# Performance work log

Hardware: AMD Instinct MI355X
Metric: run time of the kernel (lower is better)

Reference implementation:

```python
import jax, jax.numpy as jnp
import numpy as np

INF = 99999.0  # sentinel used by the original torch module


def _dtw_table(x, y):
    """Full (N+1, M+1) DTW DP table, identical math to the torch double loop.

    Row recurrence: r[j+1] = c[j] + min(prev[j+1], prev[j], r[j]).
    Rewritten as the min-plus linear recurrence r[j+1] = min(a[j] + r[j], b[j])
    with a[j] = c[j], b[j] = c[j] + min(prev[j+1], prev[j]), which is
    associative and solved per-row with lax.associative_scan (wavefront-free
    parallelism within each row); rows advance with lax.scan.
    """
    M = y.shape[0]
    dt = x.dtype
    row0 = jnp.full((M + 1,), INF, dtype=dt).at[0].set(0.0)  # dtw[0, :]
    inf1 = jnp.full((1,), INF, dtype=dt)

    def combine(l, r):
        a1, b1 = l
        a2, b2 = r
        return (a1 + a2, jnp.minimum(a2 + b1, b2))

    def step(prev, xi):
        c = (xi - y) ** 2                              # (M,) squared cost
        m = jnp.minimum(prev[1:], prev[:-1])           # min(dtw[i,j+1], dtw[i,j])
        A, B = jax.lax.associative_scan(combine, (c, c + m))
        r = jnp.minimum(A + INF, B)                    # r[0] = INF folded in
        row = jnp.concatenate([inf1, r])               # dtw[i+1, :]
        return row, row

    _, rows = jax.lax.scan(step, row0, x)              # (N, M+1)
    table = jnp.concatenate([row0[None, :], rows], axis=0)
    return jnp.sqrt(table)


def setup_inputs() -> dict:
    key = jax.random.key(0)
    kx, ky = jax.random.split(key)
    N = M = 6144
    x = jax.random.normal(kx, (N,), dtype=jnp.float32)
    y = jax.random.normal(ky, (M,), dtype=jnp.float32)
    return {"x": x, "y": y}


def reference(x, y):
    return _dtw_table(x, y)
```

## Files before the change

kernel.cpp:

```cpp
#include <hip/hip_runtime.h>
#include <math.h>

#define NN    6144
#define MP1   6145
#define FINF  99999.0f

#define R1     8
#define KC1    8
#define WCH1   (KC1 * 64)
#define GCH1   (NN / WCH1)
#define RTS1   8
#define NWS1   (NN / R1)
#define STEPS1 (NWS1 + 63)

#define R2     4
#define KC2    8
#define WCH2   (KC2 * 64)
#define BR     192
#define NBI    (NN / BR)
#define TS2    (BR / R2)
#define STEPS2 (TS2 + 63)

typedef float f4a __attribute__((ext_vector_type(4), aligned(4)));
typedef float f4v __attribute__((ext_vector_type(4), aligned(16)));

__device__ __forceinline__ float readlane_f(float v, int l) {
    return __int_as_float(__builtin_amdgcn_readlane(__float_as_int(v), l));
}
__device__ __forceinline__ float shup1(float v) {
    return __int_as_float(__builtin_amdgcn_update_dpp(
        0, __float_as_int(v), 0x138, 0xF, 0xF, false));
}

__global__ void __launch_bounds__(64, 1) dtw_bnd(const float* __restrict__ x,
                                                 const float* __restrict__ y,
                                                 int* __restrict__ flags,
                                                 float* __restrict__ bnd,
                                                 float* __restrict__ rowb) {
    const int g    = blockIdx.x;
    const int lane = threadIdx.x;
    const int c0   = g * WCH1 + lane * KC1;

    float yv[KC1], cur[KC1];
#pragma unroll
    for (int q = 0; q < KC1; ++q) {
        yv[q]  = y[c0 + q];
        cur[q] = FINF;
    }
    float pl = (c0 == 0) ? 0.0f : FINF;
    float rowval[R1];
#pragma unroll
    for (int r = 0; r < R1; ++r) rowval[r] = FINF;
    float vbuf = FINF, vnext = FINF;

    const float4* x4 = (const float4*)x;
    float4 xwA  = x4[2 * lane];
    float4 xwB  = x4[2 * lane + 1];
    float4 xwAN = x4[2 * (64 + lane)];
    float4 xwBN = x4[2 * (64 + lane) + 1];
    float xcur[R1];
#pragma unroll
    for (int r = 0; r < R1; ++r) xcur[r] = x[r];

    if (g != 0) {
        while (__hip_atomic_load(&flags[(g - 1) * 16], __ATOMIC_ACQUIRE,
                                 __HIP_MEMORY_SCOPE_AGENT) < 1) {
            __builtin_amdgcn_s_sleep(1);
        }
        vnext = bnd[(size_t)(g - 1) * NN + lane];
    }

    for (int s = 0; s < STEPS1; ++s) {
        if (g != GCH1 - 1 && s > 64 && ((s - 64) & (RTS1 - 1)) == 0) {
            if (lane == 0)
                __hip_atomic_store(&flags[g * 16], (s - 64) >> 3,
                                   __ATOMIC_RELEASE, __HIP_MEMORY_SCOPE_AGENT);
        }

        if (g != 0 && s < NWS1 && (s & (RTS1 - 1)) == 0) vbuf = vnext;

        if (g != 0 && (s & (RTS1 - 1)) == RTS1 - 4 && (s + 4) < NWS1) {
            const int want = ((s + 4) >> 3) + 1;
            while (__hip_atomic_load(&flags[(g - 1) * 16], __ATOMIC_ACQUIRE,
                                     __HIP_MEMORY_SCOPE_AGENT) < want) {
                __builtin_amdgcn_s_sleep(1);
            }
            vnext = bnd[(size_t)(g - 1) * NN + (size_t)R1 * (s + 4) + lane];
        }

        float vin[R1];
#pragma unroll
        for (int r = 0; r < R1; ++r) {
            const float up = shup1(rowval[r]);
            const float vb = readlane_f(vbuf, ((s & (RTS1 - 1)) << 3) + r);
            const float l0 = (g == 0) ? FINF : vb;
            vin[r] = (lane == 0) ? l0 : up;
        }

        const int  t      = s - lane;
        const bool active = (t >= 0) && (t < NWS1);
        if (active) {
            float rv[R1], rd[R1];
#pragma unroll
            for (int r = 0; r < R1; ++r) rv[r] = vin[r];

#pragma unroll
            for (int d = 0; d < R1 + KC1 - 1; ++d) {
#pragma unroll
                for (int r = R1 - 1; r >= 0; --r) {
                    const int q = d - r;
                    if (q < 0 || q >= KC1) continue;
                    const float up = (r == 0) ? cur[q] : rv[r - 1];
                    const float dg = (r == 0) ? ((q == 0) ? pl : cur[q - 1])
                                              : rd[r - 1];
                    const float dx = xcur[r] - yv[q];
                    const float nv = dx * dx + fminf(fminf(up, dg), rv[r]);
                    rd[r] = rv[r];
                    rv[r] = nv;
                    if (r == R1 - 1) cur[q] = nv;
                }
            }
#pragma unroll
            for (int r = 0; r < R1; ++r) rowval[r] = rv[r];
            pl = vin[R1 - 1];

            {
                const int tp1 = t + 1;
                const int k   = tp1 / 24;
                if (k * 24 == tp1 && k >= 1 && k <= NBI - 1) {
                    *(f4a*)&rowb[(size_t)k * MP1 + c0 + 1] =
                        (f4a){cur[0], cur[1], cur[2], cur[3]};
                    *(f4a*)&rowb[(size_t)k * MP1 + c0 + 5] =
                        (f4a){cur[4], cur[5], cur[6], cur[7]};
                }
            }
            if (lane == 63) {
                *(f4v*)&bnd[(size_t)g * NN + (size_t)R1 * t] =
                    (f4v){rowval[0], rowval[1], rowval[2], rowval[3]};
                *(f4v*)&bnd[(size_t)g * NN + (size_t)R1 * t + 4] =
                    (f4v){rowval[4], rowval[5], rowval[6], rowval[7]};
            }
        }

        const int sn = s + 1;
        if ((sn & 63) == 0) {
            xwA = xwAN;
            xwB = xwBN;
            int nb = sn + 64 + lane;
            if (nb > NN / 8 - 1) nb = NN / 8 - 1;
            xwAN = x4[2 * nb];
            xwBN = x4[2 * nb + 1];
        }
        const float* xap = (const float*)&xwA;
        const float* xbp = (const float*)&xwB;
#pragma unroll
        for (int r = 0; r < 4; ++r) {
            const float xs = shup1(xcur[r]);
            const float xj = readlane_f(xap[r], sn & 63);
            xcur[r] = (lane == 0) ? xj : xs;
        }
#pragma unroll
        for (int r = 4; r < 8; ++r) {
            const float xs = shup1(xcur[r]);
            const float xj = readlane_f(xbp[r - 4], sn & 63);
            xcur[r] = (lane == 0) ? xj : xs;
        }
    }

    if (g != GCH1 - 1 && lane == 0) {
        __hip_atomic_store(&flags[g * 16], NWS1 >> 3,
                           __ATOMIC_RELEASE, __HIP_MEMORY_SCOPE_AGENT);
    }
}

__global__ void __launch_bounds__(64, 1) dtw_tile(const float* __restrict__ x,
                                                  const float* __restrict__ y,
                                                  const float* __restrict__ bnd,
                                                  const float* __restrict__ rowb,
                                                  float* __restrict__ out) {
    const int bj   = blockIdx.x;
    const int bi   = blockIdx.y;
    const int lane = threadIdx.x;

    __shared__ float left_s[BR];
    __shared__ float top_s[WCH2 + 1];
    __shared__ float xb_s[BR];

#pragma unroll
    for (int k = 0; k < BR / 64; ++k) {
        const int i = 64 * k + lane;
        left_s[i] = (bj == 0) ? FINF
                              : bnd[(size_t)(bj - 1) * NN + BR * bi + i];
        xb_s[i] = x[BR * bi + i];
    }
    for (int c = lane; c < WCH2 + 1; c += 64) {
        float tv;
        if (bi == 0)                tv = (bj == 0 && c == 0) ? 0.0f : FINF;
        else if (c == 0 && bj == 0) tv = FINF;
        else                        tv = rowb[(size_t)bi * MP1 + WCH2 * bj + c];
        top_s[c] = tv;
    }
    __syncthreads();

    const int c0 = WCH2 * bj + KC2 * lane;
    float yv[KC2], cur[KC2];
#pragma unroll
    for (int q = 0; q < KC2; ++q) {
        yv[q]  = y[c0 + q];
        cur[q] = top_s[KC2 * lane + q + 1];
    }
    float pl = top_s[KC2 * lane];
    float rlast[R2];
#pragma unroll
    for (int r = 0; r < R2; ++r) rlast[r] = FINF;

    float xcur[R2];
#pragma unroll
    for (int r = 0; r < R2; ++r) xcur[r] = xb_s[r];

    int off = (BR * bi + 1 - R2 * lane) * MP1 + c0 + 1;

    for (int s = 0; s < STEPS2; ++s) {
        float vin[R2];
#pragma unroll
        for (int r = 0; r < R2; ++r) {
            const float up = shup1(rlast[r]);
            const int  li  = R2 * s + r;
            const float l0 = left_s[li < BR ? li : BR - 1];
            vin[r] = (lane == 0) ? l0 : up;
        }

        const int  t      = s - lane;
        const bool active = (t >= 0) && (t < TS2);
        if (active) {
            float rv[R2], rd[R2], nvm[R2][KC2];
#pragma unroll
            for (int r = 0; r < R2; ++r) rv[r] = vin[r];

#pragma unroll
            for (int d = 0; d < R2 + KC2 - 1; ++d) {
#pragma unroll
                for (int r = R2 - 1; r >= 0; --r) {
                    const int q = d - r;
                    if (q < 0 || q >= KC2) continue;
                    const float up = (r == 0) ? cur[q] : rv[r - 1];
                    const float dg = (r == 0) ? ((q == 0) ? pl : cur[q - 1])
                                              : rd[r - 1];
                    const float dx = xcur[r] - yv[q];
                    const float nv = dx * dx + fminf(fminf(up, dg), rv[r]);
                    rd[r] = rv[r];
                    rv[r] = nv;
                    nvm[r][q] = nv;
                    if (r == R2 - 1) cur[q] = nv;
                }
            }
#pragma unroll
            for (int r = 0; r < R2; ++r) rlast[r] = rv[r];
            pl = vin[R2 - 1];

#pragma unroll
            for (int r = 0; r < R2; ++r) {
                *(f4a*)(&out[off + r * MP1]) =
                    (f4a){__builtin_amdgcn_sqrtf(nvm[r][0]),
                          __builtin_amdgcn_sqrtf(nvm[r][1]),
                          __builtin_amdgcn_sqrtf(nvm[r][2]),
                          __builtin_amdgcn_sqrtf(nvm[r][3])};
                *(f4a*)(&out[off + r * MP1 + 4]) =
                    (f4a){__builtin_amdgcn_sqrtf(nvm[r][4]),
                          __builtin_amdgcn_sqrtf(nvm[r][5]),
                          __builtin_amdgcn_sqrtf(nvm[r][6]),
                          __builtin_amdgcn_sqrtf(nvm[r][7])};
            }
        }
        off += R2 * MP1;

        const int sn = s + 1;
#pragma unroll
        for (int r = 0; r < R2; ++r) {
            const float xs = shup1(xcur[r]);
            const int  xi  = R2 * sn + r;
            const float xj = xb_s[xi < BR ? xi : BR - 1];
            xcur[r] = (lane == 0) ? xj : xs;
        }
    }
}

__global__ void dtw_edges(float* __restrict__ out, float ev) {
    const int idx = blockIdx.x * blockDim.x + threadIdx.x;
    if (idx <= NN) {
        out[idx] = (idx == 0) ? 0.0f : ev;
        if (idx >= 1) out[(size_t)idx * MP1] = ev;
    }
}

extern "C" void kernel_launch(void* const* d_in, const int* in_sizes, int n_in,
                              void* d_out, int out_size, void* d_ws, size_t ws_size,
                              hipStream_t stream) {
    (void)in_sizes; (void)n_in; (void)out_size; (void)ws_size;
    const float* x = (const float*)d_in[0];
    const float* y = (const float*)d_in[1];
    float* out     = (float*)d_out;
    int* flags     = (int*)d_ws;

    const size_t bnd_off  = 4096;
    const size_t bnd_sz   = (size_t)GCH1 * NN * sizeof(float);
    const size_t rowb_off = bnd_off + bnd_sz;
    float* bnd  = (float*)((char*)d_ws + bnd_off);
    float* rowb = (float*)((char*)d_ws + rowb_off);

    hipMemsetAsync(flags, 0, GCH1 * 16 * sizeof(int), stream);

    dtw_edges<<<(MP1 + 255) / 256, 256, 0, stream>>>(out, sqrtf(FINF));
    dtw_bnd<<<GCH1, 64, 0, stream>>>(x, y, flags, bnd, rowb);
    dtw_tile<<<dim3(GCH1, NBI), 64, 0, stream>>>(x, y, bnd, rowb, out);
}
```

Before: 1.686 ms.

## Feed wavefront boundary and x values via DPP rotation, cache flags, peel loop

Boundary values and x samples are now held per lane in registers and fed to lane 0 through a DPP row shift that uses the rotated value as the old operand. This replaces the readlane, select and LDS lookups on each step of both kernels. The producer flag is now cached and prefetched a few steps early to cut atomic polling, and the main loop is peeled so the steady-state middle section skips the active-lane check. It relies on the DPP row-rotate semantics being correct across the whole wave and adds register pressure.

```diff
diff --git a/kernel.cpp b/kernel.cpp
--- a/kernel.cpp
+++ b/kernel.cpp
@@ -9,7 +9,6 @@
 #define KC1    8
 #define WCH1   (KC1 * 64)
 #define GCH1   (NN / WCH1)
-#define RTS1   8
 #define NWS1   (NN / R1)
 #define STEPS1 (NWS1 + 63)
 
@@ -24,19 +23,21 @@
 typedef float f4a __attribute__((ext_vector_type(4), aligned(4)));
 typedef float f4v __attribute__((ext_vector_type(4), aligned(16)));
 
-__device__ __forceinline__ float readlane_f(float v, int l) {
-    return __int_as_float(__builtin_amdgcn_readlane(__float_as_int(v), l));
-}
-__device__ __forceinline__ float shup1(float v) {
+__device__ __forceinline__ float shr1_old(float old, float v) {
     return __int_as_float(__builtin_amdgcn_update_dpp(
-        0, __float_as_int(v), 0x138, 0xF, 0xF, false));
-}
-
-__global__ void __launch_bounds__(64, 1) dtw_bnd(const float* __restrict__ x,
-                                                 const float* __restrict__ y,
-                                                 int* __restrict__ flags,
-                                                 float* __restrict__ bnd,
-                                                 float* __restrict__ rowb) {
+        __float_as_int(old), __float_as_int(v), 0x138, 0xF, 0xF, false));
+}
+__device__ __forceinline__ float rot_dn(float v) {
+    return __int_as_float(__builtin_amdgcn_update_dpp(
+        0, __float_as_int(v), 0x130, 0xF, 0xF, false));
+}
+
+__global__ __launch_bounds__(64) __attribute__((amdgpu_waves_per_eu(1, 1)))
+void dtw_bnd(const float* __restrict__ x,
+             const float* __restrict__ y,
+             int* __restrict__ flags,
+             float* __restrict__ bnd,
+             float* __restrict__ rowb) {
     const int g    = blockIdx.x;
     const int lane = threadIdx.x;
     const int c0   = g * WCH1 + lane * KC1;
@@ -51,54 +52,68 @@
     float rowval[R1];
 #pragma unroll
     for (int r = 0; r < R1; ++r) rowval[r] = FINF;
-    float vbuf = FINF, vnext = FINF;
-
-    const float4* x4 = (const float4*)x;
-    float4 xwA  = x4[2 * lane];
-    float4 xwB  = x4[2 * lane + 1];
-    float4 xwAN = x4[2 * (64 + lane)];
-    float4 xwBN = x4[2 * (64 + lane) + 1];
-    float xcur[R1];
-#pragma unroll
-    for (int r = 0; r < R1; ++r) xcur[r] = x[r];
+
+    float vrow[R1], vnrow[R1];
+#pragma unroll
+    for (int r = 0; r < R1; ++r) { vrow[r] = FINF; vnrow[r] = FINF; }
+
+    float xcur[R1], xrow[R1];
+#pragma unroll
+    for (int r = 0; r < R1; ++r) {
+        xcur[r] = x[r];
+        int tt = lane + 1; if (tt > NWS1 - 1) tt = NWS1 - 1;
+        xrow[r] = x[(tt << 3) + r];
+    }
+
+    int fcache = 0;
 
     if (g != 0) {
-        while (__hip_atomic_load(&flags[(g - 1) * 16], __ATOMIC_ACQUIRE,
-                                 __HIP_MEMORY_SCOPE_AGENT) < 1) {
+        while ((fcache = __hip_atomic_load(&flags[(g - 1) * 16], __ATOMIC_ACQUIRE,
+                                           __HIP_MEMORY_SCOPE_AGENT)) < 1) {
             __builtin_amdgcn_s_sleep(1);
         }
-        vnext = bnd[(size_t)(g - 1) * NN + lane];
-    }
-
-    for (int s = 0; s < STEPS1; ++s) {
-        if (g != GCH1 - 1 && s > 64 && ((s - 64) & (RTS1 - 1)) == 0) {
+        const float* bb = bnd + (size_t)(g - 1) * NN;
+#pragma unroll
+        for (int r = 0; r < R1; ++r) vnrow[r] = bb[(lane << 3) + r];
+    }
+
+    auto step = [&](const int s, const bool chk) {
+        if (g != GCH1 - 1 && s > 64 && ((s - 64) & 7) == 0) {
             if (lane == 0)
                 __hip_atomic_store(&flags[g * 16], (s - 64) >> 3,
                                    __ATOMIC_RELEASE, __HIP_MEMORY_SCOPE_AGENT);
         }
-
-        if (g != 0 && s < NWS1 && (s & (RTS1 - 1)) == 0) vbuf = vnext;
-
-        if (g != 0 && (s & (RTS1 - 1)) == RTS1 - 4 && (s + 4) < NWS1) {
+        if (s < NWS1 && (s & 7) == 0) {
+#pragma unroll
+            for (int r = 0; r < R1; ++r) vrow[r] = vnrow[r];
+        }
+        if (g != 0 && (s & 7) == 2 && (s + 6) < NWS1) {
+            const int want = ((s + 6) >> 3) + 1;
+            if (fcache < want)
+                fcache = __hip_atomic_load(&flags[(g - 1) * 16], __ATOMIC_ACQUIRE,
+                                           __HIP_MEMORY_SCOPE_AGENT);
+        }
+        if (g != 0 && (s & 7) == 4 && (s + 4) < NWS1) {
             const int want = ((s + 4) >> 3) + 1;
-            while (__hip_atomic_load(&flags[(g - 1) * 16], __ATOMIC_ACQUIRE,
-                                     __HIP_MEMORY_SCOPE_AGENT) < want) {
-                __builtin_amdgcn_s_sleep(1);
-            }
-            vnext = bnd[(size_t)(g - 1) * NN + (size_t)R1 * (s + 4) + lane];
+            while (fcache < want) {
+                fcache = __hip_atomic_load(&flags[(g - 1) * 16], __ATOMIC_ACQUIRE,
+                                           __HIP_MEMORY_SCOPE_AGENT);
+                if (fcache < want) __builtin_amdgcn_s_sleep(1);
+            }
+            const float* bb = bnd + (size_t)(g - 1) * NN + ((size_t)(s + 4) << 3);
+#pragma unroll
+            for (int r = 0; r < R1; ++r) vnrow[r] = bb[(lane << 3) + r];
         }
 
         float vin[R1];
 #pragma unroll
         for (int r = 0; r < R1; ++r) {
-            const float up = shup1(rowval[r]);
-            const float vb = readlane_f(vbuf, ((s & (RTS1 - 1)) << 3) + r);
-            const float l0 = (g == 0) ? FINF : vb;
-            vin[r] = (lane == 0) ? l0 : up;
+            vin[r]  = shr1_old(vrow[r], rowval[r]);
+            vrow[r] = rot_dn(vrow[r]);
         }
 
         const int  t      = s - lane;
-        const bool active = (t >= 0) && (t < NWS1);
+        const bool active = chk ? (t >= 0 && t < NWS1) : true;
         if (active) {
             float rv[R1], rd[R1];
 #pragma unroll
@@ -144,28 +159,22 @@
 
         const int sn = s + 1;
         if ((sn & 63) == 0) {
-            xwA = xwAN;
-            xwB = xwBN;
-            int nb = sn + 64 + lane;
-            if (nb > NN / 8 - 1) nb = NN / 8 - 1;
-            xwAN = x4[2 * nb];
-            xwBN = x4[2 * nb + 1];
-        }
-        const float* xap = (const float*)&xwA;
-        const float* xbp = (const float*)&xwB;
-#pragma unroll
-        for (int r = 0; r < 4; ++r) {
-            const float xs = shup1(xcur[r]);
-            const float xj = readlane_f(xap[r], sn & 63);
-            xcur[r] = (lane == 0) ? xj : xs;
-        }
-#pragma unroll
-        for (int r = 4; r < 8; ++r) {
-            const float xs = shup1(xcur[r]);
-            const float xj = readlane_f(xbp[r - 4], sn & 63);
-            xcur[r] = (lane == 0) ? xj : xs;
-        }
-    }
+#pragma unroll
+            for (int r = 0; r < R1; ++r) {
+                int tt = sn + lane; if (tt > NWS1 - 1) tt = NWS1 - 1;
+                xrow[r] = x[(tt << 3) + r];
+            }
+        }
+#pragma unroll
+        for (int r = 0; r < R1; ++r) {
+            xcur[r] = shr1_old(xrow[r], xcur[r]);
+            xrow[r] = rot_dn(xrow[r]);
+        }
+    };
+
+    for (int s = 0; s < 63; ++s)          step(s, true);
+    for (int s = 63; s < NWS1; ++s)       step(s, false);
+    for (int s = NWS1; s < STEPS1; ++s)   step(s, true);
 
     if (g != GCH1 - 1 && lane == 0) {
         __hip_atomic_store(&flags[g * 16], NWS1 >> 3,
@@ -173,26 +182,17 @@
     }
 }
 
-__global__ void __launch_bounds__(64, 1) dtw_tile(const float* __restrict__ x,
-                                                  const float* __restrict__ y,
-                                                  const float* __restrict__ bnd,
-                                                  const float* __restrict__ rowb,
-                                                  float* __restrict__ out) {
+__global__ __launch_bounds__(64) __attribute__((amdgpu_waves_per_eu(1, 1)))
+void dtw_tile(const float* __restrict__ x,
+              const float* __restrict__ y,
+              const float* __restrict__ bnd,
+              const float* __restrict__ rowb,
+              float* __restrict__ out) {
     const int bj   = blockIdx.x;
     const int bi   = blockIdx.y;
     const int lane = threadIdx.x;
 
-    __shared__ float left_s[BR];
     __shared__ float top_s[WCH2 + 1];
-    __shared__ float xb_s[BR];
-
-#pragma unroll
-    for (int k = 0; k < BR / 64; ++k) {
-        const int i = 64 * k + lane;
-        left_s[i] = (bj == 0) ? FINF
-                              : bnd[(size_t)(bj - 1) * NN + BR * bi + i];
-        xb_s[i] = x[BR * bi + i];
-    }
     for (int c = lane; c < WCH2 + 1; c += 64) {
         float tv;
         if (bi == 0)                tv = (bj == 0 && c == 0) ? 0.0f : FINF;
@@ -200,6 +200,22 @@
         else                        tv = rowb[(size_t)bi * MP1 + WCH2 * bj + c];
         top_s[c] = tv;
     }
+
+    float lrow[R2];
+    const float* lb = bnd + (size_t)(bj - 1) * NN + (size_t)BR * bi;
+#pragma unroll
+    for (int r = 0; r < R2; ++r) {
+        int li = 4 * lane + r; if (li > BR - 1) li = BR - 1;
+        lrow[r] = (bj == 0) ? FINF : lb[li];
+    }
+    float xcur[R2], xr2[R2];
+    const float* xb = x + BR * bi;
+#pragma unroll
+    for (int r = 0; r < R2; ++r) {
+        xcur[r] = xb[r];
+        int xi = 4 * (lane + 1) + r; if (xi > BR - 1) xi = BR - 1;
+        xr2[r] = xb[xi];
+    }
     __syncthreads();
 
     const int c0 = WCH2 * bj + KC2 * lane;
@@ -214,20 +230,14 @@
 #pragma unroll
     for (int r = 0; r < R2; ++r) rlast[r] = FINF;
 
-    float xcur[R2];
-#pragma unroll
-    for (int r = 0; r < R2; ++r) xcur[r] = xb_s[r];
-
     int off = (BR * bi + 1 - R2 * lane) * MP1 + c0 + 1;
 
     for (int s = 0; s < STEPS2; ++s) {
         float vin[R2];
 #pragma unroll
         for (int r = 0; r < R2; ++r) {
-            const float up = shup1(rlast[r]);
-            const int  li  = R2 * s + r;
-            const float l0 = left_s[li < BR ? li : BR - 1];
-            vin[r] = (lane == 0) ? l0 : up;
+            vin[r]  = shr1_old(lrow[r], rlast[r]);
+            lrow[r] = rot_dn(lrow[r]);
         }
 
         const int  t      = s - lane;
@@ -274,13 +284,10 @@
         }
         off += R2 * MP1;
 
-        const int sn = s + 1;
 #pragma unroll
         for (int r = 0; r < R2; ++r) {
-            const float xs = shup1(xcur[r]);
-            const int  xi  = R2 * sn + r;
-            const float xj = xb_s[xi < BR ? xi : BR - 1];
-            xcur[r] = (lane == 0) ? xj : xs;
+            xcur[r] = shr1_old(xr2[r], xcur[r]);
+            xr2[r]  = rot_dn(xr2[r]);
         }
     }
 }
```

New measurement: 1.498 ms. -11.2%, faster.
